# Optimization experiments

Measured on AMD Instinct MI355X. Metric: run time of the kernel, lower is better.

## Reference

```python
import jax, jax.numpy as jnp
import numpy as np


def setup_inputs() -> dict:
    key = jax.random.key(0)
    k1, k2 = jax.random.split(key)
    B, D1, D2 = 32768, 1024, 4096
    g1 = jax.random.normal(k1, (B, D1), dtype=jnp.float32)
    # Learned parameter, initialized as in the module: N(0,1)*0.02 + 0.2
    W = jax.random.normal(k2, (D1, D2), dtype=jnp.float32) * 0.02 + 0.2
    return {"g1": g1, "W": W}


def reference(g1, W):
    beta = 10.0
    # Column-normalize W: each column divided by its L2 norm. [d1, d2]
    nc = jnp.sqrt(jnp.sum(W ** 2, axis=0, keepdims=True))
    nW = W / nc
    # Similarity scores. [B, d2]
    x2 = g1 @ nW
    # Scaled logsumexp energy. [B]
    return -1.0 / beta * jax.nn.logsumexp(beta * x2, axis=-1)
```

## Files before the change

### kernel.cpp

```cpp
#include <hip/hip_runtime.h>
#include <hip/hip_bf16.h>
#include <hip/hip_fp8.h>

typedef int i32x8 __attribute__((ext_vector_type(8)));
typedef int i32x4 __attribute__((ext_vector_type(4)));
typedef float f32x4 __attribute__((ext_vector_type(4)));
typedef unsigned char uchar_t;

constexpr int NB = 32768;
constexpr int D1 = 1024;
constexpr int D2 = 4096;
constexpr float BETA_LOG2E = 14.4269504088896340736f;
constexpr float SCALE_A = 16.0f;
constexpr float SCALE_B = 8192.0f;
constexpr float INV_SCALE = 1.0f / (16.0f * 8192.0f);

__device__ __forceinline__ uchar_t f32_to_fp8(float f) {
  __hip_fp8_e4m3 q(f);
  return (uchar_t)q.__x;
}

__device__ __forceinline__ void async_copy16(const void* g, void* l) {
  __builtin_amdgcn_global_load_lds(
      (const __attribute__((address_space(1))) void*)g,
      (__attribute__((address_space(3))) void*)l, 16, 0, 0);
}

__global__ void colstats(const float* __restrict__ W, float* __restrict__ sq,
                         float* __restrict__ colsum) {
  int j = blockIdx.x * 256 + threadIdx.x;
  int k0 = blockIdx.y * 64;
  float a = 0.f, b = 0.f;
#pragma unroll 8
  for (int k = 0; k < 64; ++k) {
    float w = W[(size_t)(k0 + k) * D2 + j];
    a += w * w; b += w;
  }
  atomicAdd(&sq[j], a);
  atomicAdd(&colsum[j], b);
}

__global__ void convert_a(const float* __restrict__ g1, uchar_t* __restrict__ A8,
                          float* __restrict__ S) {
  int row = blockIdx.x;
  int t = threadIdx.x;
  const float* src = g1 + (size_t)row * D1 + t * 8;
  float v[8];
  *(float4*)(v)     = *(const float4*)(src);
  *(float4*)(v + 4) = *(const float4*)(src + 4);
  float sum = 0.f;
  union { uchar_t b[8]; uint2 u; } o;
#pragma unroll
  for (int j = 0; j < 8; ++j) { sum += v[j]; o.b[j] = f32_to_fp8(v[j] * SCALE_A); }
  *(uint2*)(A8 + (size_t)row * D1 + t * 8) = o.u;
#pragma unroll
  for (int m = 1; m < 64; m <<= 1) sum += __shfl_xor(sum, m, 64);
  __shared__ float part[2];
  if ((t & 63) == 0) part[t >> 6] = sum;
  __syncthreads();
  if (t == 0) S[row] = part[0] + part[1];
}

__global__ void convert_b(const float* __restrict__ W, const float* __restrict__ sq,
                          const float* __restrict__ colsum,
                          uchar_t* __restrict__ B8t, float* __restrict__ mu) {
  __shared__ float tile[64][65];
  int t = threadIdx.x;
  int j0 = blockIdx.x * 64;
  int k0 = blockIdx.y * 64;
  int c = t & 63, r4 = t >> 6;
#pragma unroll
  for (int s = 0; s < 16; ++s) {
    int k = s * 4 + r4;
    tile[k][c] = W[(size_t)(k0 + k) * D2 + j0 + c];
  }
  __syncthreads();
#pragma unroll
  for (int s = 0; s < 16; ++s) {
    int jj = s * 4 + r4;
    float inv = 1.0f / sqrtf(sq[j0 + jj]);
    float muj = colsum[j0 + jj] * inv * (1.0f / 1024.0f);
    if (k0 == 0 && c == 0) mu[j0 + jj] = muj;
    float dw = tile[c][jj] * inv - muj;
    B8t[(size_t)(j0 + jj) * D1 + k0 + c] = f32_to_fp8(dw * SCALE_B);
  }
}

__global__ __launch_bounds__(256, 4)
void gemm_expsum(const uchar_t* __restrict__ A8, const uchar_t* __restrict__ B8t,
                 const float* __restrict__ S, const float* __restrict__ mu,
                 float* __restrict__ s) {
  __shared__ __align__(16) uchar_t As[128 * 128];
  __shared__ __align__(16) uchar_t Bs[128 * 128];

  const int t = threadIdx.x;
  const int row0 = blockIdx.y * 128;
  const int col0 = blockIdx.x * 128;
  const int lane = t & 63;
  const int wave = t >> 6;
  const int wm = (wave >> 1) * 64;
  const int wn = (wave & 1) * 64;
  const int llo = lane & 15, lhi = lane >> 4;

  f32x4 acc[4][4] = {};

  const int srow = t >> 3;
  const int sseg = (t & 7) ^ (srow & 7);
  const uchar_t* gA = A8  + (size_t)(row0 + srow) * D1 + sseg * 16;
  const uchar_t* gB = B8t + (size_t)(col0 + srow) * D1 + sseg * 16;
  uchar_t* lA = As + t * 16;
  uchar_t* lB = Bs + t * 16;

  union Frag { i32x8 v; i32x4 h[2]; };

  for (int kt = 0; kt < D1; kt += 128) {
#pragma unroll
    for (int i = 0; i < 4; ++i) {
      async_copy16(gA + (size_t)i * 32 * D1 + kt, lA + i * 4096);
      async_copy16(gB + (size_t)i * 32 * D1 + kt, lB + i * 4096);
    }
    __syncthreads();

    const int sw0 = ((lhi * 2 + 0) ^ (llo & 7)) * 16;
    const int sw1 = ((lhi * 2 + 1) ^ (llo & 7)) * 16;
    Frag af[4], bq[4];
#pragma unroll
    for (int mi = 0; mi < 4; ++mi) {
      const uchar_t* p = As + (wm + mi * 16 + llo) * 128;
      af[mi].h[0] = *(const i32x4*)(p + sw0);
      af[mi].h[1] = *(const i32x4*)(p + sw1);
    }
#pragma unroll
    for (int ni = 0; ni < 4; ++ni) {
      const uchar_t* p = Bs + (wn + ni * 16 + llo) * 128;
      bq[ni].h[0] = *(const i32x4*)(p + sw0);
      bq[ni].h[1] = *(const i32x4*)(p + sw1);
    }
#pragma unroll
    for (int mi = 0; mi < 4; ++mi)
#pragma unroll
      for (int ni = 0; ni < 4; ++ni)
        acc[mi][ni] = __builtin_amdgcn_mfma_scale_f32_16x16x128_f8f6f4(
            af[mi].v, bq[ni].v, acc[mi][ni],
            0, 0,
            0, 127,
            0, 127);
    __syncthreads();
  }

  float muv[4];
#pragma unroll
  for (int ni = 0; ni < 4; ++ni) muv[ni] = mu[col0 + wn + ni * 16 + llo];

#pragma unroll
  for (int mi = 0; mi < 4; ++mi) {
    const int row = row0 + wm + mi * 16 + lhi * 4;
    float4 sv = *(const float4*)(S + row);
    float sarr[4] = {sv.x, sv.y, sv.z, sv.w};
    float rs[4];
#pragma unroll
    for (int r = 0; r < 4; ++r) {
      float v = 0.f;
#pragma unroll
      for (int ni = 0; ni < 4; ++ni) {
        float x2 = fmaf(acc[mi][ni][r], INV_SCALE, muv[ni] * sarr[r]);
        v += exp2f(x2 * BETA_LOG2E);
      }
      rs[r] = v;
    }
#pragma unroll
    for (int m = 1; m < 16; m <<= 1) {
#pragma unroll
      for (int r = 0; r < 4; ++r)
        rs[r] += __shfl_xor(rs[r], m, 64);
    }
    if (llo == 0) {
#pragma unroll
      for (int r = 0; r < 4; ++r)
        atomicAdd(&s[row + r], rs[r]);
    }
  }
}

__global__ void finish_kernel(const float* __restrict__ s, float* __restrict__ out) {
  int b = blockIdx.x * 256 + threadIdx.x;
  out[b] = -0.1f * logf(s[b]);
}

extern "C" void kernel_launch(void* const* d_in, const int* in_sizes, int n_in,
                              void* d_out, int out_size, void* d_ws, size_t ws_size,
                              hipStream_t stream) {
  const float* g1 = (const float*)d_in[0];
  const float* W  = (const float*)d_in[1];
  float* out = (float*)d_out;

  char* ws = (char*)d_ws;
  float* s       = (float*)ws;
  float* sq      = (float*)(ws + 131072);
  float* colsum  = (float*)(ws + 147456);
  float* mu      = (float*)(ws + 163840);
  float* S       = (float*)(ws + 180224);
  uchar_t* A8    = (uchar_t*)(ws + 311296);
  uchar_t* B8t   = (uchar_t*)(ws + 311296 + 33554432);

  hipMemsetAsync(ws, 0, 180224, stream);

  colstats<<<dim3(16, 16), 256, 0, stream>>>(W, sq, colsum);
  convert_b<<<dim3(64, 16), 256, 0, stream>>>(W, sq, colsum, B8t, mu);
  convert_a<<<dim3(32768), 128, 0, stream>>>(g1, A8, S);
  gemm_expsum<<<dim3(32, 256), 256, 0, stream>>>(A8, B8t, S, mu, s);
  finish_kernel<<<dim3(128), 256, 0, stream>>>(s, out);
}
```

Baseline: 505.5 us.

## Double-buffer LDS tiles in fp8 GEMM to overlap loads with MFMA

Adds a second LDS buffer for the A and B tiles. The next K-tile is prefetched with global_load_lds while the current tile is consumed, and the loop now needs one barrier per iteration instead of two. LDS use doubles to 64KB per block, so launch bounds drop from 4 to 2 blocks per CU, which lowers occupancy. Fragment packing now uses shufflevector instead of a union.

```diff
diff --git a/kernel.cpp b/kernel.cpp
--- a/kernel.cpp
+++ b/kernel.cpp
@@ -86,12 +86,12 @@
   }
 }
 
-__global__ __launch_bounds__(256, 4)
+__global__ __launch_bounds__(256, 2)
 void gemm_expsum(const uchar_t* __restrict__ A8, const uchar_t* __restrict__ B8t,
                  const float* __restrict__ S, const float* __restrict__ mu,
                  float* __restrict__ s) {
-  __shared__ __align__(16) uchar_t As[128 * 128];
-  __shared__ __align__(16) uchar_t Bs[128 * 128];
+  __shared__ __align__(16) uchar_t As[2 * 128 * 128];
+  __shared__ __align__(16) uchar_t Bs[2 * 128 * 128];
 
   const int t = threadIdx.x;
   const int row0 = blockIdx.y * 128;
@@ -108,44 +108,54 @@
   const int sseg = (t & 7) ^ (srow & 7);
   const uchar_t* gA = A8  + (size_t)(row0 + srow) * D1 + sseg * 16;
   const uchar_t* gB = B8t + (size_t)(col0 + srow) * D1 + sseg * 16;
-  uchar_t* lA = As + t * 16;
-  uchar_t* lB = Bs + t * 16;
-
-  union Frag { i32x8 v; i32x4 h[2]; };
-
-  for (int kt = 0; kt < D1; kt += 128) {
-#pragma unroll
-    for (int i = 0; i < 4; ++i) {
-      async_copy16(gA + (size_t)i * 32 * D1 + kt, lA + i * 4096);
-      async_copy16(gB + (size_t)i * 32 * D1 + kt, lB + i * 4096);
-    }
+
+  const int sw0 = ((lhi * 2 + 0) ^ (llo & 7)) * 16;
+  const int sw1 = ((lhi * 2 + 1) ^ (llo & 7)) * 16;
+
+#pragma unroll
+  for (int i = 0; i < 4; ++i) {
+    async_copy16(gA + (size_t)i * 32 * D1, As + t * 16 + i * 4096);
+    async_copy16(gB + (size_t)i * 32 * D1, Bs + t * 16 + i * 4096);
+  }
+
+  int p = 0;
+  for (int kt = 0; kt < D1; kt += 128, p ^= 1) {
     __syncthreads();
-
-    const int sw0 = ((lhi * 2 + 0) ^ (llo & 7)) * 16;
-    const int sw1 = ((lhi * 2 + 1) ^ (llo & 7)) * 16;
-    Frag af[4], bq[4];
+    if (kt + 128 < D1) {
+#pragma unroll
+      for (int i = 0; i < 4; ++i) {
+        async_copy16(gA + (size_t)i * 32 * D1 + kt + 128,
+                     As + (p ^ 1) * 16384 + t * 16 + i * 4096);
+        async_copy16(gB + (size_t)i * 32 * D1 + kt + 128,
+                     Bs + (p ^ 1) * 16384 + t * 16 + i * 4096);
+      }
+    }
+    const uchar_t* baseA = As + p * 16384;
+    const uchar_t* baseB = Bs + p * 16384;
+    i32x8 af[4], bq[4];
 #pragma unroll
     for (int mi = 0; mi < 4; ++mi) {
-      const uchar_t* p = As + (wm + mi * 16 + llo) * 128;
-      af[mi].h[0] = *(const i32x4*)(p + sw0);
-      af[mi].h[1] = *(const i32x4*)(p + sw1);
+      const uchar_t* q = baseA + (wm + mi * 16 + llo) * 128;
+      i32x4 h0 = *(const i32x4*)(q + sw0);
+      i32x4 h1 = *(const i32x4*)(q + sw1);
+      af[mi] = __builtin_shufflevector(h0, h1, 0, 1, 2, 3, 4, 5, 6, 7);
     }
 #pragma unroll
     for (int ni = 0; ni < 4; ++ni) {
-      const uchar_t* p = Bs + (wn + ni * 16 + llo) * 128;
-      bq[ni].h[0] = *(const i32x4*)(p + sw0);
-      bq[ni].h[1] = *(const i32x4*)(p + sw1);
+      const uchar_t* q = baseB + (wn + ni * 16 + llo) * 128;
+      i32x4 h0 = *(const i32x4*)(q + sw0);
+      i32x4 h1 = *(const i32x4*)(q + sw1);
+      bq[ni] = __builtin_shufflevector(h0, h1, 0, 1, 2, 3, 4, 5, 6, 7);
     }
 #pragma unroll
     for (int mi = 0; mi < 4; ++mi)
 #pragma unroll
       for (int ni = 0; ni < 4; ++ni)
         acc[mi][ni] = __builtin_amdgcn_mfma_scale_f32_16x16x128_f8f6f4(
-            af[mi].v, bq[ni].v, acc[mi][ni],
+            af[mi], bq[ni], acc[mi][ni],
             0, 0,
             0, 127,
             0, 127);
-    __syncthreads();
   }
 
   float muv[4];
```

After: 421.6 us. -16.6%, faster.
